# Optimization experiments

Hardware: AMD Instinct MI355X
Metric: run time of the kernel (lower is better)

## Reference

```python
import jax, jax.numpy as jnp
import numpy as np
import math

B, S, DIM = 1, 2048, 1024
H, KVH = 16, 4
HD = DIM // H            # 64
KV_DIM = KVH * HD        # 256


def setup_inputs() -> dict:
    key = jax.random.key(0)
    ks = jax.random.split(key, 8)
    std = 0.02
    return {
        "x": jax.random.normal(ks[0], (B, S, DIM), jnp.float32),
        "Wq": jax.random.normal(ks[1], (DIM, DIM), jnp.float32) * std,
        "Wk": jax.random.normal(ks[2], (KV_DIM, DIM), jnp.float32) * std,
        "Wv": jax.random.normal(ks[3], (KV_DIM, DIM), jnp.float32) * std,
        "Wg": jax.random.normal(ks[4], (KV_DIM, DIM), jnp.float32) * std,
        "Wo": jax.random.normal(ks[5], (DIM, DIM), jnp.float32) * std,
        "q_gain": jnp.full((H,), 1.0, jnp.float32),
        "lambda_param": jnp.full((H,), 0.5, jnp.float32),
    }


def _rms_norm(x):
    eps = jnp.finfo(x.dtype).eps
    return x * jax.lax.rsqrt(jnp.mean(x * x, axis=-1, keepdims=True) + eps)


def _polar_rotary(seq_len, head_dim, dtype):
    # PolarRotary: angles = arange(0, d, 2)/d * pi; radius decays with position
    angles = jnp.arange(0, head_dim, 2, dtype=jnp.float32) / head_dim * math.pi
    pos = jnp.arange(seq_len, dtype=jnp.float32)
    radius = 1.0 / (1.0 + pos[:, None] * 0.01)          # [S, 1]
    ang = pos[:, None] * angles[None, :]                 # [S, d/2]
    cos = (radius * jnp.cos(ang)).astype(dtype)          # [S, d/2]
    sin = (radius * jnp.sin(ang)).astype(dtype)
    return cos[None, None], sin[None, None]              # [1,1,S,d/2]


def _apply_rotary(x, cos, sin):
    half = x.shape[-1] // 2
    x1, x2 = x[..., :half], x[..., half:]
    return jnp.concatenate([x1 * cos + x2 * sin, x1 * -sin + x2 * cos], axis=-1)


def _causal_attn(q, k, v, scale, mask):
    # q,k,v: [B,H,S,d]
    s = jnp.einsum("bhqd,bhkd->bhqk", q, k) * scale
    s = jnp.where(mask, s, jnp.finfo(s.dtype).min)
    p = jax.nn.softmax(s, axis=-1)
    return jnp.einsum("bhqk,bhkd->bhqd", p, v)


def reference(x, Wq, Wk, Wv, Wg, Wo, q_gain, lambda_param):
    bsz, seqlen, dim = x.shape
    q = (x @ Wq.T).reshape(bsz, seqlen, H, HD).transpose(0, 2, 1, 3)      # [B,H,S,d]
    k = (x @ Wk.T).reshape(bsz, seqlen, KVH, HD).transpose(0, 2, 1, 3)    # [B,KVH,S,d]
    v = (x @ Wv.T).reshape(bsz, seqlen, KVH, HD).transpose(0, 2, 1, 3)

    # value gate (VGA)
    v_g = jax.nn.sigmoid((x @ Wg.T).reshape(bsz, seqlen, KVH, HD).transpose(0, 2, 1, 3))
    v = v * v_g

    q = _rms_norm(q)
    k = _rms_norm(k)

    cos, sin = _polar_rotary(seqlen, HD, q.dtype)
    q = _apply_rotary(q, cos, sin)
    k = _apply_rotary(k, cos, sin)

    q = q * q_gain.astype(q.dtype)[None, :, None, None]

    # GQA: repeat kv heads
    rep = H // KVH
    k = jnp.repeat(k, rep, axis=1)
    v = jnp.repeat(v, rep, axis=1)

    # differential attention: split head dim in halves
    half = HD // 2
    q1, q2 = q[..., :half], q[..., half:]
    k1, k2 = k[..., :half], k[..., half:]
    v1, v2 = v[..., :half], v[..., half:]

    scale = 1.0 / math.sqrt(half)
    mask = jnp.tril(jnp.ones((seqlen, seqlen), dtype=bool))[None, None]
    a1 = _causal_attn(q1, k1, v1, scale, mask)
    a2 = _causal_attn(q2, k2, v2, scale, mask)

    lp = lambda_param.astype(q.dtype)[None, :, None, None]
    y = jnp.concatenate([a1 - lp * a2, a1 + lp * a2], axis=-1)            # [B,H,S,d]
    y = y.transpose(0, 2, 1, 3).reshape(bsz, seqlen, dim)
    return y @ Wo.T
```

## Files before the change

kernel.cpp:

```cpp
#include <hip/hip_runtime.h>
#include <hip/hip_bf16.h>
#include <math.h>

#define S_LEN 2048
#define DIM   1024
#define NH    16
#define NKVH  4
#define HD    64
#define KVDIM 256

typedef __hip_bfloat16 bf16;
typedef __attribute__((ext_vector_type(8))) short short8;
typedef __attribute__((ext_vector_type(4))) float f32x4;

#define GLOBAL_AS __attribute__((address_space(1)))
#define LDS_AS    __attribute__((address_space(3)))

__device__ __forceinline__ void gload_lds16(const bf16* g, bf16* l) {
    __builtin_amdgcn_global_load_lds((const GLOBAL_AS void*)g, (LDS_AS void*)l,
                                     16, 0, 0);
}

__global__ __launch_bounds__(256) void cast6(
    const float* __restrict__ x,  const float* __restrict__ Wq,
    const float* __restrict__ Wk, const float* __restrict__ Wv,
    const float* __restrict__ Wg, const float* __restrict__ Wo,
    bf16* __restrict__ xb,  bf16* __restrict__ Wqb,
    bf16* __restrict__ Wkb, bf16* __restrict__ Wvb,
    bf16* __restrict__ Wgb, bf16* __restrict__ Wob,
    float* __restrict__ rc, float* __restrict__ rs,
    const float* __restrict__ lp) {
    if (blockIdx.y == 6) {
        const int idx = blockIdx.x * 256 + threadIdx.x;
        if (idx < S_LEN * 32) {
            const int s = idx >> 5, i = idx & 31;
            float af  = (float)(((double)(2 * i) / 64.0) * 3.14159265358979323846);
            float ang = (float)s * af;
            float radius = 1.0f / (1.0f + 0.01f * (float)s);
            rc[idx] = radius * (float)cos((double)ang);
            rs[idx] = radius * (float)sin((double)ang);
        }
        return;
    }
    if (blockIdx.y == 5) {
        for (int i = (blockIdx.x * 256 + threadIdx.x) * 4; i < DIM * DIM;
             i += gridDim.x * 1024) {
            const int n = i >> 10, c = i & (DIM - 1);
            const int h = c >> 6, half = (c >> 5) & 1, d = c & 31;
            const float* base = Wo + (size_t)n * DIM + h * 64 + d;
            float4 w1 = *(const float4*)(base);
            float4 w2 = *(const float4*)(base + 32);
            const float lam = lp[h];
            float4 r;
            if (half == 0) {
                r.x = w1.x + w2.x; r.y = w1.y + w2.y;
                r.z = w1.z + w2.z; r.w = w1.w + w2.w;
            } else {
                r.x = lam * (w2.x - w1.x); r.y = lam * (w2.y - w1.y);
                r.z = lam * (w2.z - w1.z); r.w = lam * (w2.w - w1.w);
            }
            Wob[i]     = __float2bfloat16(r.x);
            Wob[i + 1] = __float2bfloat16(r.y);
            Wob[i + 2] = __float2bfloat16(r.z);
            Wob[i + 3] = __float2bfloat16(r.w);
        }
        return;
    }
    const float* s; bf16* d; int n;
    switch (blockIdx.y) {
        case 0: s = x;  d = xb;  n = S_LEN * DIM; break;
        case 1: s = Wq; d = Wqb; n = DIM * DIM;   break;
        case 2: s = Wk; d = Wkb; n = KVDIM * DIM; break;
        case 3: s = Wv; d = Wvb; n = KVDIM * DIM; break;
        default: s = Wg; d = Wgb; n = KVDIM * DIM; break;
    }
    for (int i = (blockIdx.x * 256 + threadIdx.x) * 4; i < n; i += gridDim.x * 1024) {
        float4 v = *(const float4*)(s + i);
        d[i]     = __float2bfloat16(v.x);
        d[i + 1] = __float2bfloat16(v.y);
        d[i + 2] = __float2bfloat16(v.z);
        d[i + 3] = __float2bfloat16(v.w);
    }
}

__device__ __forceinline__ void gemm_core(
    const bf16* __restrict__ A, const bf16* __restrict__ B,
    float* __restrict__ C, int bm, int bn, int N, int K) {
    __shared__ bf16 As[64 * 64];
    __shared__ bf16 Bs[64 * 64];
    const int tid  = threadIdx.x;
    const int w    = tid >> 6;
    const int lane = tid & 63;
    const int quad = lane >> 4;
    const int lm   = lane & 15;
    const int srow = tid >> 3;
    const int sseg = (tid & 7) ^ (srow & 7);
    const bf16* a0p = A + (size_t)(bm + srow) * K + (sseg << 3);
    const bf16* a1p = a0p + (size_t)32 * K;
    const bf16* b0p = B + (size_t)(bn + srow) * K + (sseg << 3);
    const bf16* b1p = b0p + (size_t)32 * K;
    bf16* ldsA = As + w * 512;
    bf16* ldsB = Bs + w * 512;

    f32x4 acc[4] = {};
    const int ra  = w * 16 + lm;
    const int rax = ra & 7;
    const int aoff0 = ra * 64 + (((quad    ) ^ rax) << 3);
    const int aoff1 = ra * 64 + (((quad + 4) ^ rax) << 3);
    const int rbx = lm & 7;
    const int boff0 = lm * 64 + (((quad    ) ^ rbx) << 3);
    const int boff1 = lm * 64 + (((quad + 4) ^ rbx) << 3);

    for (int k0 = 0; k0 < K; k0 += 64) {
        gload_lds16(a0p + k0, ldsA);
        gload_lds16(a1p + k0, ldsA + 2048);
        gload_lds16(b0p + k0, ldsB);
        gload_lds16(b1p + k0, ldsB + 2048);
        __syncthreads();
        short8 a0 = *(const short8*)&As[aoff0];
        short8 a1 = *(const short8*)&As[aoff1];
        #pragma unroll
        for (int t = 0; t < 4; ++t) {
            short8 b0 = *(const short8*)&Bs[boff0 + t * 16 * 64];
            short8 b1 = *(const short8*)&Bs[boff1 + t * 16 * 64];
            acc[t] = __builtin_amdgcn_mfma_f32_16x16x32_bf16(a0, b0, acc[t], 0, 0, 0);
            acc[t] = __builtin_amdgcn_mfma_f32_16x16x32_bf16(a1, b1, acc[t], 0, 0, 0);
        }
        __syncthreads();
    }
    const int r0 = bm + w * 16 + quad * 4;
    #pragma unroll
    for (int t = 0; t < 4; ++t) {
        const int col = bn + t * 16 + lm;
        #pragma unroll
        for (int i = 0; i < 4; ++i)
            C[(size_t)(r0 + i) * N + col] = acc[t][i];
    }
}

__global__ __launch_bounds__(256) void gemm_out(
    const bf16* __restrict__ Yb, const bf16* __restrict__ Wob,
    float* __restrict__ C) {
    gemm_core(Yb, Wob, C, blockIdx.y * 64, blockIdx.x * 64, DIM, DIM);
}

__global__ __launch_bounds__(256) void gemm_qkvg_post(
    const bf16* __restrict__ xb,  const bf16* __restrict__ Wqb,
    const bf16* __restrict__ Wkb, const bf16* __restrict__ Wvb,
    const bf16* __restrict__ Wgb,
    bf16* __restrict__ Qb, bf16* __restrict__ Kpk, bf16* __restrict__ Vpk,
    const float* __restrict__ qgain,
    const float* __restrict__ rc, const float* __restrict__ rs) {
    __shared__ bf16 As[64 * 64];
    __shared__ bf16 Bs[64 * 64];
    __shared__ bf16 Gs[64 * 64];
    const int cx = blockIdx.x;
    const int bm = blockIdx.y * 64;
    const int tid  = threadIdx.x;
    const int w    = tid >> 6;
    const int lane = tid & 63;
    const int quad = lane >> 4;
    const int lm   = lane & 15;
    const int srow = tid >> 3;
    const int sseg = (tid & 7) ^ (srow & 7);

    int mode, bn;
    const bf16 *B0, *B1;
    if (cx < 4)      { mode = 2; bn = cx * 64;        B0 = Wvb; B1 = Wgb; }
    else if (cx < 8) { mode = 1; bn = (cx - 4) * 64;  B0 = Wkb; B1 = Wkb; }
    else             { mode = 0; bn = (cx - 8) * 64;  B0 = Wqb; B1 = Wqb; }

    const bf16* a0p = xb + (size_t)(bm + srow) * DIM + (sseg << 3);
    const bf16* a1p = a0p + (size_t)32 * DIM;
    const bf16* b0p = B0 + (size_t)(bn + srow) * DIM + (sseg << 3);
    const bf16* b1p = b0p + (size_t)32 * DIM;
    const bf16* g0p = B1 + (size_t)(bn + srow) * DIM + (sseg << 3);
    const bf16* g1p = g0p + (size_t)32 * DIM;
    bf16* ldsA = As + w * 512;
    bf16* ldsB = Bs + w * 512;
    bf16* ldsG = Gs + w * 512;

    f32x4 acc[4]  = {};
    f32x4 acc2[4] = {};
    const int ra  = w * 16 + lm;
    const int rax = ra & 7;
    const int aoff0 = ra * 64 + (((quad    ) ^ rax) << 3);
    const int aoff1 = ra * 64 + (((quad + 4) ^ rax) << 3);
    const int rbx = lm & 7;
    const int boff0 = lm * 64 + (((quad    ) ^ rbx) << 3);
    const int boff1 = lm * 64 + (((quad + 4) ^ rbx) << 3);

    for (int k0 = 0; k0 < DIM; k0 += 64) {
        gload_lds16(a0p + k0, ldsA);
        gload_lds16(a1p + k0, ldsA + 2048);
        gload_lds16(b0p + k0, ldsB);
        gload_lds16(b1p + k0, ldsB + 2048);
        if (mode == 2) {
            gload_lds16(g0p + k0, ldsG);
            gload_lds16(g1p + k0, ldsG + 2048);
        }
        __syncthreads();
        short8 a0 = *(const short8*)&As[aoff0];
        short8 a1 = *(const short8*)&As[aoff1];
        #pragma unroll
        for (int t = 0; t < 4; ++t) {
            short8 b0 = *(const short8*)&Bs[boff0 + t * 16 * 64];
            short8 b1 = *(const short8*)&Bs[boff1 + t * 16 * 64];
            acc[t] = __builtin_amdgcn_mfma_f32_16x16x32_bf16(a0, b0, acc[t], 0, 0, 0);
            acc[t] = __builtin_amdgcn_mfma_f32_16x16x32_bf16(a1, b1, acc[t], 0, 0, 0);
        }
        if (mode == 2) {
            #pragma unroll
            for (int t = 0; t < 4; ++t) {
                short8 g0 = *(const short8*)&Gs[boff0 + t * 16 * 64];
                short8 g1 = *(const short8*)&Gs[boff1 + t * 16 * 64];
                acc2[t] = __builtin_amdgcn_mfma_f32_16x16x32_bf16(a0, g0, acc2[t], 0, 0, 0);
                acc2[t] = __builtin_amdgcn_mfma_f32_16x16x32_bf16(a1, g1, acc2[t], 0, 0, 0);
            }
        }
        __syncthreads();
    }

    const int r0 = bm + w * 16 + quad * 4;
    if (mode == 2) {
        const int kvh = cx;
        #pragma unroll
        for (int t = 0; t < 4; ++t) {
            const int d = t * 16 + lm;
            const int half = d >> 5, d32 = d & 31;
            #pragma unroll
            for (int i = 0; i < 4; ++i) {
                const int s = r0 + i;
                float val = acc[t][i] / (1.0f + __expf(-acc2[t][i]));
                const size_t vi = (((((size_t)(kvh*2 + half)*64 + (s>>5))*2 + (d32>>4))*64)
                                   + ((s&31)>>3)*16 + (d32&15))*8 + (s&7);
                Vpk[vi] = __float2bfloat16(val);
            }
        }
    } else {
        const float gain = (mode == 0) ? qgain[cx - 8] : 1.0f;
        float rr[4];
        #pragma unroll
        for (int i = 0; i < 4; ++i) {
            float v0 = acc[0][i] * acc[0][i] + acc[2][i] * acc[2][i];
            float v1 = acc[1][i] * acc[1][i] + acc[3][i] * acc[3][i];
            float ssv = v0 + v1;
            ssv += __shfl_xor(ssv, 8);
            ssv += __shfl_xor(ssv, 4);
            ssv += __shfl_xor(ssv, 2);
            ssv += __shfl_xor(ssv, 1);
            rr[i] = rsqrtf(ssv * (1.0f/64.0f) + 1.1920928955078125e-7f);
        }
        #pragma unroll
        for (int t = 0; t < 4; ++t) {
            const int d = t * 16 + lm;
            #pragma unroll
            for (int i = 0; i < 4; ++i) {
                const int s = r0 + i;
                float n  = acc[t][i]     * rr[i];
                float no = acc[t ^ 2][i] * rr[i];
                const int ri = s * 32 + (d & 31);
                float c = rc[ri], sn = rs[ri];
                float val = (t < 2) ? (n * c + no * sn) * gain
                                    : (n * c + -no * sn) * gain;
                if (mode == 0) {
                    Qb[(size_t)s * DIM + (cx - 8) * 64 + d] = __float2bfloat16(val);
                } else {
                    const int kvh = cx - 4;
                    const int half = d >> 5, d32 = d & 31;
                    const size_t ki = (((((size_t)(kvh*2 + half)*64 + (s>>5))*2 + ((s&31)>>4))*64)
                                       + (d32>>3)*16 + (s&15))*8 + (d32&7);
                    Kpk[ki] = __float2bfloat16(val);
                }
            }
        }
    }
}

__global__ __launch_bounds__(256, 8) void attn_mfma(
    const bf16* __restrict__ Qb, const bf16* __restrict__ Kpk,
    const bf16* __restrict__ Vpk, bf16* __restrict__ Yab) {
    __shared__ short PW[4][640];
    __shared__ float RED[3][64][13];
    const int id    = blockIdx.x;
    const int qtile = 127 - (id >> 5);
    const int hh    = id & 31;
    const int h     = hh >> 1;
    const int half  = hh & 1;
    const int kvh   = h >> 2;
    const int tid   = threadIdx.x;
    const int wid   = tid >> 6;
    const int lane  = tid & 63;
    const int quad  = lane >> 4;
    const int m     = lane & 15;
    bf16* PWb = (bf16*)PW[wid];

    const int qrow = qtile * 16 + m;
    short8 qf = *(const short8*)(Qb + (size_t)qrow * DIM + h * HD + half * 32 + quad * 8);

    const bf16* kbase = Kpk + (size_t)(kvh * 2 + half) * 64 * 1024 + lane * 8;
    const bf16* vbase = Vpk + (size_t)(kvh * 2 + half) * 64 * 1024 + lane * 8;

    f32x4 o0 = {}, o1 = {};
    float lpart[4] = {0.f, 0.f, 0.f, 0.f};
    const float scale = 0.17677669529663687f;
    const int rbase = qtile * 16 + quad * 4;
    const int nkt = (qtile >> 1) + 1;

    for (int kb = wid; kb < nkt; kb += 4) {
        short8 kf0 = *(const short8*)(kbase + kb * 1024);
        short8 kf1 = *(const short8*)(kbase + kb * 1024 + 512);
        f32x4 s0 = {}, s1 = {};
        __builtin_amdgcn_s_setprio(1);
        s0 = __builtin_amdgcn_mfma_f32_16x16x32_bf16(qf, kf0, s0, 0, 0, 0);
        s1 = __builtin_amdgcn_mfma_f32_16x16x32_bf16(qf, kf1, s1, 0, 0, 0);
        __builtin_amdgcn_s_setprio(0);
        short8 vt0 = *(const short8*)(vbase + kb * 1024);
        short8 vt1 = *(const short8*)(vbase + kb * 1024 + 512);

        float p0v[4], p1v[4];
        if (kb * 32 + 31 <= qtile * 16) {
            #pragma unroll
            for (int r = 0; r < 4; ++r) {
                p0v[r] = __expf(s0[r] * scale);
                p1v[r] = __expf(s1[r] * scale);
            }
        } else {
            const int kg = kb * 32 + m;
            #pragma unroll
            for (int r = 0; r < 4; ++r) {
                const int rg = rbase + r;
                p0v[r] = (kg > rg)      ? 0.f : __expf(s0[r] * scale);
                p1v[r] = (kg + 16 > rg) ? 0.f : __expf(s1[r] * scale);
            }
        }
        #pragma unroll
        for (int r = 0; r < 4; ++r) {
            lpart[r] += p0v[r] + p1v[r];
            PWb[(quad * 4 + r) * 40 + m]      = __float2bfloat16(p0v[r]);
            PWb[(quad * 4 + r) * 40 + 16 + m] = __float2bfloat16(p1v[r]);
        }
        asm volatile("s_waitcnt lgkmcnt(0)" ::: "memory");
        short8 pf = *(const short8*)&PW[wid][m * 40 + quad * 8];
        __builtin_amdgcn_s_setprio(1);
        o0 = __builtin_amdgcn_mfma_f32_16x16x32_bf16(pf, vt0, o0, 0, 0, 0);
        o1 = __builtin_amdgcn_mfma_f32_16x16x32_bf16(pf, vt1, o1, 0, 0, 0);
        __builtin_amdgcn_s_setprio(0);
    }

    if (wid > 0) {
        float* rp = &RED[wid - 1][lane][0];
        #pragma unroll
        for (int r = 0; r < 4; ++r) {
            rp[r]     = o0[r];
            rp[4 + r] = o1[r];
            rp[8 + r] = lpart[r];
        }
    }
    __syncthreads();
    if (wid == 0) {
        #pragma unroll
        for (int wv = 0; wv < 3; ++wv) {
            const float* rp = &RED[wv][lane][0];
            #pragma unroll
            for (int r = 0; r < 4; ++r) {
                o0[r]     += rp[r];
                o1[r]     += rp[4 + r];
                lpart[r]  += rp[8 + r];
            }
        }
        #pragma unroll
        for (int r = 0; r < 4; ++r) {
            float v = lpart[r];
            v += __shfl_xor(v, 1);
            v += __shfl_xor(v, 2);
            v += __shfl_xor(v, 4);
            v += __shfl_xor(v, 8);
            lpart[r] = 1.f / v;
        }
        #pragma unroll
        for (int r = 0; r < 4; ++r) {
            bf16* op = Yab + (size_t)(rbase + r) * DIM + h * HD + half * 32;
            op[m]      = __float2bfloat16(o0[r] * lpart[r]);
            op[16 + m] = __float2bfloat16(o1[r] * lpart[r]);
        }
    }
}

extern "C" void kernel_launch(void* const* d_in, const int* in_sizes, int n_in,
                              void* d_out, int out_size, void* d_ws, size_t ws_size,
                              hipStream_t stream) {
    const float* x  = (const float*)d_in[0];
    const float* Wq = (const float*)d_in[1];
    const float* Wk = (const float*)d_in[2];
    const float* Wv = (const float*)d_in[3];
    const float* Wg = (const float*)d_in[4];
    const float* Wo = (const float*)d_in[5];
    const float* qg = (const float*)d_in[6];
    const float* lp = (const float*)d_in[7];
    float* out = (float*)d_out;

    char* ws = (char*)d_ws;
    bf16* Qb   = (bf16*)ws;
    bf16* Kpk  = (bf16*)(ws + (8u << 20));
    bf16* Vpk  = (bf16*)(ws + (9u << 20));
    float* rc  = (float*)(ws + (14u << 20));
    float* rs  = (float*)(ws + (14u << 20) + (256u << 10));
    bf16* Yab  = (bf16*)(ws + (14u << 20));
    bf16* xb   = (bf16*)(ws + (22u << 20));
    bf16* Wqb  = (bf16*)(ws + (26u << 20));
    bf16* Wkb  = (bf16*)(ws + (28u << 20));
    bf16* Wvb  = (bf16*)(ws + (28u << 20) + (512u << 10));
    bf16* Wgb  = (bf16*)(ws + (29u << 20));
    bf16* Wob  = (bf16*)(ws + (29u << 20) + (512u << 10));

    cast6<<<dim3(512, 7), 256, 0, stream>>>(x, Wq, Wk, Wv, Wg, Wo,
                                            xb, Wqb, Wkb, Wvb, Wgb, Wob,
                                            rc, rs, lp);

    gemm_qkvg_post<<<dim3(24, S_LEN/64), 256, 0, stream>>>(
        xb, Wqb, Wkb, Wvb, Wgb, Qb, Kpk, Vpk, qg, rc, rs);

    attn_mfma<<<4096, 256, 0, stream>>>(Qb, Kpk, Vpk, Yab);

    gemm_out<<<dim3(DIM/64, S_LEN/64), 256, 0, stream>>>(Yab, Wob, out);
}
```

Measured before the change: 129.8 us.

## Use double-buffered 128x128 tiles for Q/K projection in fused QKVG GEMM

The Q and K projection blocks now use 128x128 output tiles with four waves arranged 2x2, each computing a 64x64 sub-tile. Global-to-LDS loads are double-buffered so the next K slice is fetched while MFMAs run on the current one. The V/gate blocks keep the old 64x64 single-buffered path, and the grid becomes a flat 1D launch of 160 Q/K blocks plus 128 V blocks. The larger tiles aim to raise operand reuse and hide load latency, in exchange for much more LDS (a 64 KB pool) and more accumulator registers per block, which cuts occupancy. With only 288 blocks the grid is also small relative to the CU count.

```diff
diff --git a/kernel.cpp b/kernel.cpp
--- a/kernel.cpp
+++ b/kernel.cpp
@@ -19,6 +19,12 @@
 __device__ __forceinline__ void gload_lds16(const bf16* g, bf16* l) {
     __builtin_amdgcn_global_load_lds((const GLOBAL_AS void*)g, (LDS_AS void*)l,
                                      16, 0, 0);
+}
+
+__device__ __forceinline__ void wait_stage_and_barrier() {
+    asm volatile("s_waitcnt vmcnt(0)" ::: "memory");
+    __builtin_amdgcn_s_barrier();
+    asm volatile("" ::: "memory");
 }
 
 __global__ __launch_bounds__(256) void cast6(
@@ -151,30 +157,147 @@
     bf16* __restrict__ Qb, bf16* __restrict__ Kpk, bf16* __restrict__ Vpk,
     const float* __restrict__ qgain,
     const float* __restrict__ rc, const float* __restrict__ rs) {
-    __shared__ bf16 As[64 * 64];
-    __shared__ bf16 Bs[64 * 64];
-    __shared__ bf16 Gs[64 * 64];
-    const int cx = blockIdx.x;
-    const int bm = blockIdx.y * 64;
+    __shared__ char pool[65536];
+    const int bx   = blockIdx.x;
     const int tid  = threadIdx.x;
     const int w    = tid >> 6;
     const int lane = tid & 63;
     const int quad = lane >> 4;
     const int lm   = lane & 15;
-    const int srow = tid >> 3;
-    const int sseg = (tid & 7) ^ (srow & 7);
-
-    int mode, bn;
-    const bf16 *B0, *B1;
-    if (cx < 4)      { mode = 2; bn = cx * 64;        B0 = Wvb; B1 = Wgb; }
-    else if (cx < 8) { mode = 1; bn = (cx - 4) * 64;  B0 = Wkb; B1 = Wkb; }
-    else             { mode = 0; bn = (cx - 8) * 64;  B0 = Wqb; B1 = Wqb; }
-
-    const bf16* a0p = xb + (size_t)(bm + srow) * DIM + (sseg << 3);
+    const int srow32 = tid >> 3;
+    const int sseg   = (tid & 7) ^ (srow32 & 7);
+
+    if (bx < 160) {
+        const int col = bx % 10;
+        const int bm  = (bx / 10) * 128;
+        const bool isQ = (col < 8);
+        const bf16* Bw = isQ ? Wqb : Wkb;
+        const int bn   = isQ ? col * 128 : (col - 8) * 128;
+
+        bf16* As = (bf16*)pool;
+        bf16* Bs = (bf16*)(pool + 32768);
+        const int wr = w >> 1, wc = w & 1;
+
+        const bf16* aS = xb + (size_t)(bm + srow32) * DIM + (sseg << 3);
+        const bf16* bS = Bw + (size_t)(bn + srow32) * DIM + (sseg << 3);
+        const int wo = w * 512;
+
+        f32x4 acc[4][4] = {};
+        int aoff[4][2], boff[4][2];
+        #pragma unroll
+        for (int mr = 0; mr < 4; ++mr) {
+            const int ra = wr * 64 + mr * 16 + lm, rax = ra & 7;
+            aoff[mr][0] = ra * 64 + (((quad    ) ^ rax) << 3);
+            aoff[mr][1] = ra * 64 + (((quad + 4) ^ rax) << 3);
+        }
+        #pragma unroll
+        for (int nr = 0; nr < 4; ++nr) {
+            const int rb = wc * 64 + nr * 16 + lm, rbx = rb & 7;
+            boff[nr][0] = rb * 64 + (((quad    ) ^ rbx) << 3);
+            boff[nr][1] = rb * 64 + (((quad + 4) ^ rbx) << 3);
+        }
+
+        #pragma unroll
+        for (int i = 0; i < 4; ++i) {
+            gload_lds16(aS + (size_t)(i * 32) * DIM, As + i * 2048 + wo);
+            gload_lds16(bS + (size_t)(i * 32) * DIM, Bs + i * 2048 + wo);
+        }
+        wait_stage_and_barrier();
+
+        const int nt = DIM / 64;
+        for (int t = 0; t < nt; ++t) {
+            const int cur = t & 1;
+            if (t + 1 < nt) {
+                const int k0 = (t + 1) << 6;
+                const int nb = cur ^ 1;
+                #pragma unroll
+                for (int i = 0; i < 4; ++i) {
+                    gload_lds16(aS + (size_t)(i * 32) * DIM + k0,
+                                As + nb * 8192 + i * 2048 + wo);
+                    gload_lds16(bS + (size_t)(i * 32) * DIM + k0,
+                                Bs + nb * 8192 + i * 2048 + wo);
+                }
+            }
+            const bf16* Ac = As + cur * 8192;
+            const bf16* Bc = Bs + cur * 8192;
+            #pragma unroll
+            for (int kh = 0; kh < 2; ++kh) {
+                short8 af[4], bfr[4];
+                #pragma unroll
+                for (int mr = 0; mr < 4; ++mr) af[mr]  = *(const short8*)&Ac[aoff[mr][kh]];
+                #pragma unroll
+                for (int nr = 0; nr < 4; ++nr) bfr[nr] = *(const short8*)&Bc[boff[nr][kh]];
+                #pragma unroll
+                for (int mr = 0; mr < 4; ++mr)
+                    #pragma unroll
+                    for (int nr = 0; nr < 4; ++nr)
+                        acc[mr][nr] = __builtin_amdgcn_mfma_f32_16x16x32_bf16(
+                            af[mr], bfr[nr], acc[mr][nr], 0, 0, 0);
+            }
+            if (t + 1 < nt) wait_stage_and_barrier();
+        }
+
+        const float gain = isQ ? qgain[col * 2 + wc] : 1.0f;
+        float rr[4][4];
+        #pragma unroll
+        for (int mr = 0; mr < 4; ++mr)
+            #pragma unroll
+            for (int i = 0; i < 4; ++i) {
+                float v0 = acc[mr][0][i] * acc[mr][0][i] + acc[mr][2][i] * acc[mr][2][i];
+                float v1 = acc[mr][1][i] * acc[mr][1][i] + acc[mr][3][i] * acc[mr][3][i];
+                float ssv = v0 + v1;
+                ssv += __shfl_xor(ssv, 8);
+                ssv += __shfl_xor(ssv, 4);
+                ssv += __shfl_xor(ssv, 2);
+                ssv += __shfl_xor(ssv, 1);
+                rr[mr][i] = rsqrtf(ssv * (1.0f/64.0f) + 1.1920928955078125e-7f);
+            }
+        #pragma unroll
+        for (int mr = 0; mr < 4; ++mr) {
+            const int r0 = bm + wr * 64 + mr * 16 + quad * 4;
+            #pragma unroll
+            for (int nr = 0; nr < 4; ++nr) {
+                const int d = nr * 16 + lm;
+                #pragma unroll
+                for (int i = 0; i < 4; ++i) {
+                    const int s = r0 + i;
+                    float n  = acc[mr][nr][i]     * rr[mr][i];
+                    float no = acc[mr][nr ^ 2][i] * rr[mr][i];
+                    const int ri = s * 32 + (d & 31);
+                    float c = rc[ri], sn = rs[ri];
+                    float val = (nr < 2) ? (n * c + no * sn) * gain
+                                         : (n * c + -no * sn) * gain;
+                    if (isQ) {
+                        Qb[(size_t)s * DIM + (col * 2 + wc) * 64 + d] =
+                            __float2bfloat16(val);
+                    } else {
+                        const int kvh = (col - 8) * 2 + wc;
+                        const int half = d >> 5, d32 = d & 31;
+                        const size_t ki = (((((size_t)(kvh*2 + half)*64 + (s>>5))*2
+                                             + ((s&31)>>4))*64)
+                                           + (d32>>3)*16 + (s&15))*8 + (d32&7);
+                        Kpk[ki] = __float2bfloat16(val);
+                    }
+                }
+            }
+        }
+        return;
+    }
+
+    const int idx = bx - 160;
+    const int vcx = idx >> 5;
+    const int bm  = (idx & 31) * 64;
+    const int bn  = vcx * 64;
+
+    bf16* As = (bf16*)pool;
+    bf16* Bs = (bf16*)(pool + 8192);
+    bf16* Gs = (bf16*)(pool + 16384);
+
+    const bf16* a0p = xb  + (size_t)(bm + srow32) * DIM + (sseg << 3);
     const bf16* a1p = a0p + (size_t)32 * DIM;
-    const bf16* b0p = B0 + (size_t)(bn + srow) * DIM + (sseg << 3);
+    const bf16* b0p = Wvb + (size_t)(bn + srow32) * DIM + (sseg << 3);
     const bf16* b1p = b0p + (size_t)32 * DIM;
-    const bf16* g0p = B1 + (size_t)(bn + srow) * DIM + (sseg << 3);
+    const bf16* g0p = Wgb + (size_t)(bn + srow32) * DIM + (sseg << 3);
     const bf16* g1p = g0p + (size_t)32 * DIM;
     bf16* ldsA = As + w * 512;
     bf16* ldsB = Bs + w * 512;
@@ -195,10 +318,8 @@
         gload_lds16(a1p + k0, ldsA + 2048);
         gload_lds16(b0p + k0, ldsB);
         gload_lds16(b1p + k0, ldsB + 2048);
-        if (mode == 2) {
-            gload_lds16(g0p + k0, ldsG);
-            gload_lds16(g1p + k0, ldsG + 2048);
-        }
+        gload_lds16(g0p + k0, ldsG);
+        gload_lds16(g1p + k0, ldsG + 2048);
         __syncthreads();
         short8 a0 = *(const short8*)&As[aoff0];
         short8 a1 = *(const short8*)&As[aoff1];
@@ -209,70 +330,29 @@
             acc[t] = __builtin_amdgcn_mfma_f32_16x16x32_bf16(a0, b0, acc[t], 0, 0, 0);
             acc[t] = __builtin_amdgcn_mfma_f32_16x16x32_bf16(a1, b1, acc[t], 0, 0, 0);
         }
-        if (mode == 2) {
-            #pragma unroll
-            for (int t = 0; t < 4; ++t) {
-                short8 g0 = *(const short8*)&Gs[boff0 + t * 16 * 64];
-                short8 g1 = *(const short8*)&Gs[boff1 + t * 16 * 64];
-                acc2[t] = __builtin_amdgcn_mfma_f32_16x16x32_bf16(a0, g0, acc2[t], 0, 0, 0);
-                acc2[t] = __builtin_amdgcn_mfma_f32_16x16x32_bf16(a1, g1, acc2[t], 0, 0, 0);
-            }
+        #pragma unroll
+        for (int t = 0; t < 4; ++t) {
+            short8 g0 = *(const short8*)&Gs[boff0 + t * 16 * 64];
+            short8 g1 = *(const short8*)&Gs[boff1 + t * 16 * 64];
+            acc2[t] = __builtin_amdgcn_mfma_f32_16x16x32_bf16(a0, g0, acc2[t], 0, 0, 0);
+            acc2[t] = __builtin_amdgcn_mfma_f32_16x16x32_bf16(a1, g1, acc2[t], 0, 0, 0);
         }
         __syncthreads();
     }
 
     const int r0 = bm + w * 16 + quad * 4;
-    if (mode == 2) {
-        const int kvh = cx;
-        #pragma unroll
-        for (int t = 0; t < 4; ++t) {
-            const int d = t * 16 + lm;
-            const int half = d >> 5, d32 = d & 31;
-            #pragma unroll
-            for (int i = 0; i < 4; ++i) {
-                const int s = r0 + i;
-                float val = acc[t][i] / (1.0f + __expf(-acc2[t][i]));
-                const size_t vi = (((((size_t)(kvh*2 + half)*64 + (s>>5))*2 + (d32>>4))*64)
-                                   + ((s&31)>>3)*16 + (d32&15))*8 + (s&7);
-                Vpk[vi] = __float2bfloat16(val);
-            }
-        }
-    } else {
-        const float gain = (mode == 0) ? qgain[cx - 8] : 1.0f;
-        float rr[4];
+    const int kvh = vcx;
+    #pragma unroll
+    for (int t = 0; t < 4; ++t) {
+        const int d = t * 16 + lm;
+        const int half = d >> 5, d32 = d & 31;
         #pragma unroll
         for (int i = 0; i < 4; ++i) {
-            float v0 = acc[0][i] * acc[0][i] + acc[2][i] * acc[2][i];
-            float v1 = acc[1][i] * acc[1][i] + acc[3][i] * acc[3][i];
-            float ssv = v0 + v1;
-            ssv += __shfl_xor(ssv, 8);
-            ssv += __shfl_xor(ssv, 4);
-            ssv += __shfl_xor(ssv, 2);
-            ssv += __shfl_xor(ssv, 1);
-            rr[i] = rsqrtf(ssv * (1.0f/64.0f) + 1.1920928955078125e-7f);
-        }
-        #pragma unroll
-        for (int t = 0; t < 4; ++t) {
-            const int d = t * 16 + lm;
-            #pragma unroll
-            for (int i = 0; i < 4; ++i) {
-                const int s = r0 + i;
-                float n  = acc[t][i]     * rr[i];
-                float no = acc[t ^ 2][i] * rr[i];
-                const int ri = s * 32 + (d & 31);
-                float c = rc[ri], sn = rs[ri];
-                float val = (t < 2) ? (n * c + no * sn) * gain
-                                    : (n * c + -no * sn) * gain;
-                if (mode == 0) {
-                    Qb[(size_t)s * DIM + (cx - 8) * 64 + d] = __float2bfloat16(val);
-                } else {
-                    const int kvh = cx - 4;
-                    const int half = d >> 5, d32 = d & 31;
-                    const size_t ki = (((((size_t)(kvh*2 + half)*64 + (s>>5))*2 + ((s&31)>>4))*64)
-                                       + (d32>>3)*16 + (s&15))*8 + (d32&7);
-                    Kpk[ki] = __float2bfloat16(val);
-                }
-            }
+            const int s = r0 + i;
+            float val = acc[t][i] / (1.0f + __expf(-acc2[t][i]));
+            const size_t vi = (((((size_t)(kvh*2 + half)*64 + (s>>5))*2 + (d32>>4))*64)
+                               + ((s&31)>>3)*16 + (d32&15))*8 + (s&7);
+            Vpk[vi] = __float2bfloat16(val);
         }
     }
 }
@@ -418,7 +498,7 @@
                                             xb, Wqb, Wkb, Wvb, Wgb, Wob,
                                             rc, rs, lp);
 
-    gemm_qkvg_post<<<dim3(24, S_LEN/64), 256, 0, stream>>>(
+    gemm_qkvg_post<<<dim3(288), 256, 0, stream>>>(
         xb, Wqb, Wkb, Wvb, Wgb, Qb, Kpk, Vpk, qg, rc, rs);
 
     attn_mfma<<<4096, 256, 0, stream>>>(Qb, Kpk, Vpk, Yab);
```

Result: slower. 137.5 us (+6.0%).

## Compute transposed scores and transpose P via lane shuffles instead of LDS

Applied to the files above, without the earlier changes.

The QK^T MFMA operands are swapped so each lane holds scores for one query row across four keys. The P tile can then be packed to bf16 and rearranged into the A-operand layout of the PV MFMA with cross-lane xor shuffles, which removes the LDS round trip and its waitcnt. The row-sum bookkeeping is simplified to one partial per lane and reduced across quads at the end. Launch bounds occupancy is lowered from 8 to 6, and the extra shuffles and selects add VALU work in exchange.

```diff
diff --git a/kernel.cpp b/kernel.cpp
--- a/kernel.cpp
+++ b/kernel.cpp
@@ -12,6 +12,7 @@
 typedef __hip_bfloat16 bf16;
 typedef __attribute__((ext_vector_type(8))) short short8;
 typedef __attribute__((ext_vector_type(4))) float f32x4;
+typedef __attribute__((ext_vector_type(4))) unsigned int uint4v;
 
 #define GLOBAL_AS __attribute__((address_space(1)))
 #define LDS_AS    __attribute__((address_space(3)))
@@ -19,6 +20,13 @@
 __device__ __forceinline__ void gload_lds16(const bf16* g, bf16* l) {
     __builtin_amdgcn_global_load_lds((const GLOBAL_AS void*)g, (LDS_AS void*)l,
                                      16, 0, 0);
+}
+
+__device__ __forceinline__ unsigned pack2(float a, float b) {
+    bf16 ha = __float2bfloat16(a), hb = __float2bfloat16(b);
+    unsigned ua = *reinterpret_cast<unsigned short*>(&ha);
+    unsigned ub = *reinterpret_cast<unsigned short*>(&hb);
+    return ua | (ub << 16);
 }
 
 __global__ __launch_bounds__(256) void cast6(
@@ -277,10 +285,9 @@
     }
 }
 
-__global__ __launch_bounds__(256, 8) void attn_mfma(
+__global__ __launch_bounds__(256, 6) void attn_mfma(
     const bf16* __restrict__ Qb, const bf16* __restrict__ Kpk,
     const bf16* __restrict__ Vpk, bf16* __restrict__ Yab) {
-    __shared__ short PW[4][640];
     __shared__ float RED[3][64][13];
     const int id    = blockIdx.x;
     const int qtile = 127 - (id >> 5);
@@ -293,7 +300,6 @@
     const int lane  = tid & 63;
     const int quad  = lane >> 4;
     const int m     = lane & 15;
-    bf16* PWb = (bf16*)PW[wid];
 
     const int qrow = qtile * 16 + m;
     short8 qf = *(const short8*)(Qb + (size_t)qrow * DIM + h * HD + half * 32 + quad * 8);
@@ -302,7 +308,7 @@
     const bf16* vbase = Vpk + (size_t)(kvh * 2 + half) * 64 * 1024 + lane * 8;
 
     f32x4 o0 = {}, o1 = {};
-    float lpart[4] = {0.f, 0.f, 0.f, 0.f};
+    float lsum = 0.f;
     const float scale = 0.17677669529663687f;
     const int rbase = qtile * 16 + quad * 4;
     const int nkt = (qtile >> 1) + 1;
@@ -312,8 +318,8 @@
         short8 kf1 = *(const short8*)(kbase + kb * 1024 + 512);
         f32x4 s0 = {}, s1 = {};
         __builtin_amdgcn_s_setprio(1);
-        s0 = __builtin_amdgcn_mfma_f32_16x16x32_bf16(qf, kf0, s0, 0, 0, 0);
-        s1 = __builtin_amdgcn_mfma_f32_16x16x32_bf16(qf, kf1, s1, 0, 0, 0);
+        s0 = __builtin_amdgcn_mfma_f32_16x16x32_bf16(kf0, qf, s0, 0, 0, 0);
+        s1 = __builtin_amdgcn_mfma_f32_16x16x32_bf16(kf1, qf, s1, 0, 0, 0);
         __builtin_amdgcn_s_setprio(0);
         short8 vt0 = *(const short8*)(vbase + kb * 1024);
         short8 vt1 = *(const short8*)(vbase + kb * 1024 + 512);
@@ -326,22 +332,46 @@
                 p1v[r] = __expf(s1[r] * scale);
             }
         } else {
-            const int kg = kb * 32 + m;
+            const int qg_ = qtile * 16 + m;
+            const int k0_ = kb * 32 + quad * 4;
             #pragma unroll
             for (int r = 0; r < 4; ++r) {
-                const int rg = rbase + r;
-                p0v[r] = (kg > rg)      ? 0.f : __expf(s0[r] * scale);
-                p1v[r] = (kg + 16 > rg) ? 0.f : __expf(s1[r] * scale);
-            }
-        }
-        #pragma unroll
-        for (int r = 0; r < 4; ++r) {
-            lpart[r] += p0v[r] + p1v[r];
-            PWb[(quad * 4 + r) * 40 + m]      = __float2bfloat16(p0v[r]);
-            PWb[(quad * 4 + r) * 40 + 16 + m] = __float2bfloat16(p1v[r]);
-        }
-        asm volatile("s_waitcnt lgkmcnt(0)" ::: "memory");
-        short8 pf = *(const short8*)&PW[wid][m * 40 + quad * 8];
+                p0v[r] = (k0_ + r > qg_)      ? 0.f : __expf(s0[r] * scale);
+                p1v[r] = (k0_ + 16 + r > qg_) ? 0.f : __expf(s1[r] * scale);
+            }
+        }
+        lsum += ((p0v[0] + p0v[1]) + (p0v[2] + p0v[3]))
+              + ((p1v[0] + p1v[1]) + (p1v[2] + p1v[3]));
+
+        unsigned w0 = pack2(p0v[0], p0v[1]);
+        unsigned w1 = pack2(p0v[2], p0v[3]);
+        unsigned w2 = pack2(p1v[0], p1v[1]);
+        unsigned w3 = pack2(p1v[2], p1v[3]);
+
+        unsigned v16_0 = (lane & 16) ? w0 : w2;
+        unsigned v16_1 = (lane & 16) ? w1 : w3;
+        unsigned v32_0 = (lane & 32) ? w0 : w2;
+        unsigned v32_1 = (lane & 32) ? w1 : w3;
+        unsigned v48_0 = (quad == 2) ? w0 : w2;
+        unsigned v48_1 = (quad == 2) ? w1 : w3;
+        unsigned x16_0 = (unsigned)__shfl_xor((int)v16_0, 16);
+        unsigned x16_1 = (unsigned)__shfl_xor((int)v16_1, 16);
+        unsigned x32_0 = (unsigned)__shfl_xor((int)v32_0, 32);
+        unsigned x32_1 = (unsigned)__shfl_xor((int)v32_1, 32);
+        unsigned x48_0 = (unsigned)__shfl_xor((int)v48_0, 48);
+        unsigned x48_1 = (unsigned)__shfl_xor((int)v48_1, 48);
+
+        unsigned u0 = (quad == 0) ? w0    : (quad == 1) ? x48_0
+                    : (quad == 2) ? x32_0 : x16_0;
+        unsigned u1 = (quad == 0) ? w1    : (quad == 1) ? x48_1
+                    : (quad == 2) ? x32_1 : x16_1;
+        unsigned u2 = (quad == 0) ? x16_0 : (quad == 1) ? x32_0
+                    : (quad == 2) ? x48_0 : w2;
+        unsigned u3 = (quad == 0) ? x16_1 : (quad == 1) ? x32_1
+                    : (quad == 2) ? x48_1 : w3;
+        uint4v pu = { u0, u1, u2, u3 };
+        short8 pf = *reinterpret_cast<short8*>(&pu);
+
         __builtin_amdgcn_s_setprio(1);
         o0 = __builtin_amdgcn_mfma_f32_16x16x32_bf16(pf, vt0, o0, 0, 0, 0);
         o1 = __builtin_amdgcn_mfma_f32_16x16x32_bf16(pf, vt1, o1, 0, 0, 0);
@@ -354,8 +384,8 @@
         for (int r = 0; r < 4; ++r) {
             rp[r]     = o0[r];
             rp[4 + r] = o1[r];
-            rp[8 + r] = lpart[r];
-        }
+        }
+        rp[8] = lsum;
     }
     __syncthreads();
     if (wid == 0) {
@@ -364,25 +394,22 @@
             const float* rp = &RED[wv][lane][0];
             #pragma unroll
             for (int r = 0; r < 4; ++r) {
-                o0[r]     += rp[r];
-                o1[r]     += rp[4 + r];
-                lpart[r]  += rp[8 + r];
-            }
-        }
-        #pragma unroll
-        for (int r = 0; r < 4; ++r) {
-            float v = lpart[r];
-            v += __shfl_xor(v, 1);
-            v += __shfl_xor(v, 2);
-            v += __shfl_xor(v, 4);
-            v += __shfl_xor(v, 8);
-            lpart[r] = 1.f / v;
-        }
+                o0[r] += rp[r];
+                o1[r] += rp[4 + r];
+            }
+            lsum += rp[8];
+        }
+        lsum += __shfl_xor(lsum, 16);
+        lsum += __shfl_xor(lsum, 32);
+        float linv = 1.0f / lsum;
+        float li[4];
+        #pragma unroll
+        for (int r = 0; r < 4; ++r) li[r] = __shfl(linv, quad * 4 + r);
         #pragma unroll
         for (int r = 0; r < 4; ++r) {
             bf16* op = Yab + (size_t)(rbase + r) * DIM + h * HD + half * 32;
-            op[m]      = __float2bfloat16(o0[r] * lpart[r]);
-            op[16 + m] = __float2bfloat16(o1[r] * lpart[r]);
+            op[m]      = __float2bfloat16(o0[r] * li[r]);
+            op[16 + m] = __float2bfloat16(o1[r] * li[r]);
         }
     }
 }
```

New measurement: 131.6 us. No clear change (+1.4%).
